# Optimization experiments

Measured on AMD Instinct MI355X. Metric: run time of the kernel, lower is better.

The kernel has to match this reference:

```python
import jax, jax.numpy as jnp
import numpy as np

B, H, W = 2, 64, 64
D = 256  # in_channels
EPS = 1e-5


def conv2d(x, w, pad):
    # x: NCHW, w: OIHW
    return jax.lax.conv_general_dilated(
        x, w, window_strides=(1, 1), padding=[(pad, pad), (pad, pad)],
        dimension_numbers=("NCHW", "OIHW", "NCHW"))


def code_projection(X, codewords, scale):
    # X: [B, D, H, W]; codewords: [K, D]; scale: [D, K]
    b, d = X.shape[0], X.shape[1]
    x = X.reshape(b, d, -1).transpose(0, 2, 1)              # [B, N, D]
    # residual: [B, N, D, K] (large broadcast tensor, as in the original)
    residual = (x[:, :, :, None] - codewords.T[None, None]) * scale
    Q = jax.nn.softmax(-0.5 * jnp.sum(residual ** 2, axis=2), axis=-1)  # [B, N, K]
    Z_num = jnp.einsum("bnk,bndk->bdk", Q, residual)        # sum over N
    Z_ = Z_num / Q.sum(axis=1)[:, None, :]                  # [B, D, K]
    Z = Z_ / jnp.sqrt(jnp.sum(Z_ ** 2, axis=1, keepdims=True))  # L2 over D
    return Z, Q


def graph_conv(inp, weight, gamma, beta):
    # inp: [B, D, K]
    adj = jnp.einsum("bdk,bdl->bkl", inp, inp)              # input^T @ input
    support = jnp.einsum("ij,bjk->bik", weight, inp)        # weight @ input
    out = jnp.einsum("bdk,bkl->bdl", support, adj)          # support @ adj
    out = jax.nn.relu(out)
    # BatchNorm1d (training-mode batch stats over (B, K) per channel D)
    mean = out.mean(axis=(0, 2), keepdims=True)
    var = out.var(axis=(0, 2), keepdims=True)
    return gamma[None, :, None] * (out - mean) / jnp.sqrt(var + EPS) + beta[None, :, None]


def reproj(graph, Q, h, w):
    # graph: [B, D, K], Q: [B, N, K]
    x = jnp.einsum("bdk,bnk->bdn", graph, Q)
    return x.reshape(graph.shape[0], graph.shape[1], h, w)


def branch(c, conv_w, cw, sc, gcnw, g, bta, ext_w, h, w):
    z, q = code_projection(conv2d(c, conv_w, 1), cw, sc)
    z = graph_conv(z, gcnw, g, bta)
    return conv2d(reproj(z, q, h, w), ext_w, 0) + c


def setup_inputs() -> dict:
    key = jax.random.key(0)
    keys = iter(jax.random.split(key, 64))
    nk = lambda: next(keys)
    inp = {}
    inp["c3"] = jax.random.normal(nk(), (B, 512, H, W), jnp.float32)
    inp["c4"] = jax.random.normal(nk(), (B, 512, H, W), jnp.float32)
    inp["c5"] = jax.random.normal(nk(), (B, 512, H, W), jnp.float32)
    for name, K in [("32", 32), ("16", 16), ("8", 8)]:
        inp[f"conv{name}_w"] = jax.random.normal(nk(), (256, 512, 3, 3), jnp.float32) * 0.02
        std1 = 1.0 / np.sqrt(K * D)
        inp[f"cw{name}"] = jax.random.uniform(nk(), (K, D), jnp.float32, -std1, std1)
        inp[f"sc{name}"] = jax.random.uniform(nk(), (D, K), jnp.float32, -1.0, 0.0)
        stdv = 1.0 / np.sqrt(D)
        inp[f"gcnw{name}"] = jax.random.uniform(nk(), (D, D), jnp.float32, -stdv, stdv)
        inp[f"bng{name}"] = jax.random.uniform(nk(), (D,), jnp.float32, 0.5, 1.5)
        inp[f"bnb{name}"] = jax.random.normal(nk(), (D,), jnp.float32) * 0.1
        inp[f"ext{name}_w"] = jax.random.normal(nk(), (512, 256, 1, 1), jnp.float32) * 0.05
    inp["smooth_w"] = jax.random.normal(nk(), (512, 1536, 3, 3), jnp.float32) * 0.01
    inp["smg"] = jax.random.uniform(nk(), (512,), jnp.float32, 0.5, 1.5)
    inp["smb"] = jax.random.normal(nk(), (512,), jnp.float32) * 0.1
    return inp


def reference(c3, c4, c5,
              conv32_w, cw32, sc32, gcnw32, bng32, bnb32, ext32_w,
              conv16_w, cw16, sc16, gcnw16, bng16, bnb16, ext16_w,
              conv8_w, cw8, sc8, gcnw8, bng8, bnb8, ext8_w,
              smooth_w, smg, smb):
    h, w = c3.shape[2], c3.shape[3]
    x_32 = branch(c3, conv32_w, cw32, sc32, gcnw32, bng32, bnb32, ext32_w, h, w)
    x_16 = branch(c4, conv16_w, cw16, sc16, gcnw16, bng16, bnb16, ext16_w, h, w)
    x_8 = branch(c5, conv8_w, cw8, sc8, gcnw8, bng8, bnb8, ext8_w, h, w)
    out = jnp.concatenate([x_8, x_16, x_32], axis=1)        # [B, 1536, H, W]
    out = conv2d(out, smooth_w, 1)
    # BatchNorm2d (training-mode batch stats) + ReLU
    mean = out.mean(axis=(0, 2, 3), keepdims=True)
    var = out.var(axis=(0, 2, 3), keepdims=True)
    out = smg[None, :, None, None] * (out - mean) / jnp.sqrt(var + EPS) + smb[None, :, None, None]
    return jax.nn.relu(out)
```

## Files before the change

kernel.cpp:

```cpp
#include <hip/hip_runtime.h>
#include <hip/hip_bf16.h>
#include <math.h>

#define HWN 4096
#define DCH 256
#define EPSV 1e-5f

typedef unsigned short u16;
typedef __attribute__((ext_vector_type(8))) short short8b;
typedef __attribute__((ext_vector_type(4))) float fx4;
typedef __attribute__((ext_vector_type(8))) unsigned short u16x8;

static __device__ inline u16 f2bf(float f) {
  __hip_bfloat16 h = __float2bfloat16(f);
  return *reinterpret_cast<u16*>(&h);
}
static __device__ inline float bf2f(u16 u) {
  unsigned int v = ((unsigned int)u) << 16;
  return __uint_as_float(v);
}

__global__ __launch_bounds__(256) void t_chwc3_k(const float* __restrict__ i0p,
    const float* __restrict__ i1p, const float* __restrict__ i2p,
    u16* __restrict__ out) {
  __shared__ float tl[32][257];
  const int p0 = blockIdx.x * 256, cic = blockIdx.y;
  const int z = blockIdx.z;
  const int br = z >> 1, b = z & 1;
  const float* in = (br == 0) ? i0p : ((br == 1) ? i1p : i2p);
  const int t = threadIdx.x;
  const float* ip = in + ((size_t)(b * 512 + cic * 32)) * HWN + p0;
#pragma unroll
  for (int r = 0; r < 32; ++r) tl[r][t] = ip[(size_t)r * HWN + t];
  __syncthreads();
  u16* op = out + ((size_t)((z * 16 + cic)) * HWN + p0 + t) * 32;
#pragma unroll
  for (int g = 0; g < 4; ++g) {
    u16x8 o;
#pragma unroll
    for (int j = 0; j < 8; ++j) o[j] = f2bf(tl[g * 8 + j][t]);
    *reinterpret_cast<u16x8*>(op + g * 8) = o;
  }
}

template<int CIN, int COUT>
__global__ __launch_bounds__(256) void wpack_k(const float* __restrict__ w0,
    const float* __restrict__ w1, const float* __restrict__ w2,
    u16* __restrict__ wp) {
  constexpr int NCIC = CIN / 32, NCOG = COUT / 16;
  const int br = blockIdx.y;
  const float* w = (br == 0) ? w0 : ((br == 1) ? w1 : w2);
  u16* wpb = wp + (size_t)br * 9 * NCIC * NCOG * 512;
  const int cog = blockIdx.x % NCOG, cic = blockIdx.x / NCOG;
  __shared__ float ws_[16 * 32 * 9];
  const int t = threadIdx.x;
  const float* src = w + ((size_t)(cog * 16) * CIN + cic * 32) * 9;
  for (int i = t; i < 4608; i += 256) {
    int co = i / 288, r = i % 288;
    ws_[i] = src[(size_t)co * CIN * 9 + r];
  }
  __syncthreads();
  const size_t tapstride = (size_t)NCIC * NCOG * 512;
  const size_t base = ((size_t)cic * NCOG + cog) * 512;
#pragma unroll
  for (int tap = 0; tap < 9; ++tap) {
#pragma unroll
    for (int e0 = 0; e0 < 512; e0 += 256) {
      int e = e0 + t;
      int kg = e >> 7, m = (e >> 3) & 15, j = e & 7;
      wpb[tap * tapstride + base + e] = f2bf(ws_[m * 288 + (kg * 8 + j) * 9 + tap]);
    }
  }
}

template<int CIN, int COUT, int SPLIT, int COW, int WPE, bool BF16OUT>
__global__ __launch_bounds__(256, WPE) void convlds3_k(
    const u16* __restrict__ xt, const u16* __restrict__ wp,
    void* __restrict__ outv) {
  constexpr int NCIC = CIN / 32;
  constexpr int NCO = COUT / COW;
  constexpr int NWT = COW / 16;
  constexpr int CICPS = NCIC / SPLIT;
  constexpr int NST = CICPS * 3;
  constexpr int TAPB = COW * 32;
  constexpr int WSH = TAPB / 4;
  constexpr int RNDS = WSH / 512;
  constexpr int PXS = 40;
  constexpr int AROW = 66 * PXS;
  constexpr size_t OUTEL = (size_t)2 * COUT * HWN;
  __shared__ u16 bl[3 * TAPB];
  __shared__ u16 al[6 * AROW];

  const int br = blockIdx.y;
  xt += (size_t)br * 2 * NCIC * HWN * 32;
  wp += (size_t)br * 9 * NCIC * (COUT / 16) * 512;

  int g = blockIdx.x;
  const int cpx = (int)gridDim.x >> 3;
  g = (g & 7) * cpx + (g >> 3);
  const int s = g / (32 * NCO);
  const int rem = g % (32 * NCO);
  const int rt = rem / NCO;
  const int cob = (rem % NCO) * COW;

  const int wv = threadIdx.x >> 6, lane = threadIdx.x & 63;
  const int b = (rt * 4) >> 6;
  const int h0 = (rt * 4) & 63;
  const int h = h0 + wv;
  const int m = lane & 15, kg = lane >> 4;
  const int cic0 = s * CICPS;
  const int t = threadIdx.x;

  fx4 acc[4][NWT];
#pragma unroll
  for (int i = 0; i < 4; ++i)
#pragma unroll
    for (int jn = 0; jn < NWT; ++jn) acc[i][jn] = (fx4){0.f, 0.f, 0.f, 0.f};

  const u16x8 zero16 = (u16x8){0, 0, 0, 0, 0, 0, 0, 0};
  const int lds_lane = wv * WSH + lane * 8;
  const int a_px = t >> 2, a_sl = t & 3;
  const int a_wr = (a_px + 1) * PXS + a_sl * 8;

  auto load_a = [&](int cic, u16x8* dst) {
    const u16* xc = xt + ((size_t)(b * NCIC + cic)) * HWN * 32;
#pragma unroll
    for (int r = 0; r < 6; ++r) {
      const int hl = h0 - 1 + r;
      u16x8 v = zero16;
      if ((unsigned)hl < 64u)
        v = *reinterpret_cast<const u16x8*>(xc + (size_t)hl * 2048 + t * 8);
      dst[r] = v;
    }
  };
  auto write_a = [&](const u16x8* src) {
#pragma unroll
    for (int r = 0; r < 6; ++r)
      *reinterpret_cast<u16x8*>(&al[r * AROW + a_wr]) = src[r];
  };

  if (t < 48) {
    int r = t >> 3, side = (t >> 2) & 1, sl = t & 3;
    *reinterpret_cast<u16x8*>(&al[r * AROW + (side ? 65 * PXS : 0) + sl * 8]) = zero16;
  }
  {
    u16x8 a0[6];
    load_a(cic0, a0);
    write_a(a0);
#pragma unroll
    for (int t3 = 0; t3 < 3; ++t3) {
      const u16* srcb = wp + (((size_t)t3 * NCIC + cic0) * (COUT / 16) + (cob >> 4)) * 512;
#pragma unroll
      for (int r = 0; r < RNDS; ++r)
        *reinterpret_cast<u16x8*>(&bl[t3 * TAPB + lds_lane + r * 512]) =
            *reinterpret_cast<const u16x8*>(srcb + lds_lane + r * 512);
    }
  }
  __syncthreads();

#pragma unroll 1
  for (int st = 0; st < NST; ++st) {
    const bool hasnext = (st + 1 < NST);
    const int ty = st % 3;
    const bool newcic = hasnext && (ty == 2);
    u16x8 stg[3][RNDS];
    u16x8 astg[6];
    if (hasnext) {
      const int cicn = cic0 + (st + 1) / 3, tyn = (st + 1) % 3;
#pragma unroll
      for (int t3 = 0; t3 < 3; ++t3) {
        const int tap = tyn * 3 + t3;
        const u16* srcb = wp + (((size_t)tap * NCIC + cicn) * (COUT / 16) + (cob >> 4)) * 512;
#pragma unroll
        for (int r = 0; r < RNDS; ++r)
          stg[t3][r] = *reinterpret_cast<const u16x8*>(srcb + lds_lane + r * 512);
      }
      if (newcic) load_a(cicn, astg);
    }
    const u16* arow = al + (wv + ty) * AROW + kg * 8;
#pragma unroll
    for (int tx = 0; tx < 3; ++tx) {
      short8b a[4];
#pragma unroll
      for (int mt = 0; mt < 4; ++mt)
        a[mt] = *reinterpret_cast<const short8b*>(arow + (mt * 16 + m + tx) * PXS);
      short8b bb[NWT];
#pragma unroll
      for (int nt = 0; nt < NWT; ++nt)
        bb[nt] = *reinterpret_cast<const short8b*>(&bl[tx * TAPB + nt * 512 + lane * 8]);
#pragma unroll
      for (int mt = 0; mt < 4; ++mt)
#pragma unroll
        for (int nt = 0; nt < NWT; ++nt)
          acc[mt][nt] = __builtin_amdgcn_mfma_f32_16x16x32_bf16(a[mt], bb[nt], acc[mt][nt], 0, 0, 0);
    }
    __syncthreads();
    if (hasnext) {
      if (newcic) write_a(astg);
#pragma unroll
      for (int t3 = 0; t3 < 3; ++t3)
#pragma unroll
        for (int r = 0; r < RNDS; ++r)
          *reinterpret_cast<u16x8*>(&bl[t3 * TAPB + lds_lane + r * 512]) = stg[t3][r];
      __syncthreads();
    }
  }

#pragma unroll
  for (int mt = 0; mt < 4; ++mt)
#pragma unroll
    for (int nt = 0; nt < NWT; ++nt) {
      int co = cob + nt * 16 + m;
      size_t idx = ((size_t)(b * COUT + co)) * HWN + h * 64 + mt * 16 + kg * 4;
      if (BF16OUT) {
        u16* op = (u16*)outv + (size_t)(br * SPLIT + s) * OUTEL + idx;
        ushort4 o;
        o.x = f2bf(acc[mt][nt][0]); o.y = f2bf(acc[mt][nt][1]);
        o.z = f2bf(acc[mt][nt][2]); o.w = f2bf(acc[mt][nt][3]);
        *reinterpret_cast<ushort4*>(op) = o;
      } else {
        float* op = (float*)outv + (size_t)(br * SPLIT + s) * OUTEL + idx;
        *reinterpret_cast<fx4*>(op) = acc[mt][nt];
      }
    }
}

__global__ __launch_bounds__(256) void bnall_k(const u16* __restrict__ slab,
    float* __restrict__ dout, const float* __restrict__ gm,
    const float* __restrict__ bt) {
  const int o = blockIdx.x;
  const size_t el = (size_t)2 * 512 * HWN;
  const int t = threadIdx.x;
  float y[2][2][8];
  float s = 0.f, ss = 0.f;
#pragma unroll
  for (int b = 0; b < 2; ++b)
#pragma unroll
    for (int c = 0; c < 2; ++c) {
      const size_t base = ((size_t)(b * 512 + o)) * HWN + c * 2048 + t * 8;
      u16x8 v0 = *reinterpret_cast<const u16x8*>(slab + base);
      u16x8 v1 = *reinterpret_cast<const u16x8*>(slab + el + base);
      u16x8 v2 = *reinterpret_cast<const u16x8*>(slab + 2 * el + base);
      u16x8 v3 = *reinterpret_cast<const u16x8*>(slab + 3 * el + base);
#pragma unroll
      for (int j = 0; j < 8; ++j) {
        float yv = (bf2f(v0[j]) + bf2f(v1[j])) + (bf2f(v2[j]) + bf2f(v3[j]));
        y[b][c][j] = yv; s += yv; ss = fmaf(yv, yv, ss);
      }
    }
  __shared__ float rs[4], rss[4], fin[2];
  for (int off = 32; off; off >>= 1) { s += __shfl_down(s, off); ss += __shfl_down(ss, off); }
  int lane = t & 63, wid = t >> 6;
  if (lane == 0) { rs[wid] = s; rss[wid] = ss; }
  __syncthreads();
  if (t == 0) {
    float S = rs[0] + rs[1] + rs[2] + rs[3];
    float SS = rss[0] + rss[1] + rss[2] + rss[3];
    float mean = S / (2 * HWN);
    float var = SS / (2 * HWN) - mean * mean;
    fin[0] = mean;
    fin[1] = 1.f / sqrtf(var + EPSV);
  }
  __syncthreads();
  const float mean = fin[0], giv = fin[1] * gm[o], be = bt[o];
#pragma unroll
  for (int b = 0; b < 2; ++b)
#pragma unroll
    for (int c = 0; c < 2; ++c) {
      const size_t base = ((size_t)(b * 512 + o)) * HWN + c * 2048 + t * 8;
      fx4 o0, o1;
#pragma unroll
      for (int j = 0; j < 4; ++j)
        o0[j] = fmaxf(fmaf(y[b][c][j] - mean, giv, be), 0.f);
#pragma unroll
      for (int j = 0; j < 4; ++j)
        o1[j] = fmaxf(fmaf(y[b][c][4 + j] - mean, giv, be), 0.f);
      *reinterpret_cast<fx4*>(dout + base) = o0;
      *reinterpret_cast<fx4*>(dout + base + 4) = o1;
    }
}

__global__ __launch_bounds__(256) void prep3_k(
    const float* __restrict__ sc0, const float* __restrict__ sc1, const float* __restrict__ sc2,
    const float* __restrict__ cw0, const float* __restrict__ cw1, const float* __restrict__ cw2,
    float2* __restrict__ AB, float* __restrict__ Ck) {
  const int br = blockIdx.y;
  const int K = 8 << br;
  const int k = blockIdx.x;
  if (k >= K) return;
  const float* sc = (br == 0) ? sc0 : ((br == 1) ? sc1 : sc2);
  const float* cw = (br == 0) ? cw0 : ((br == 1) ? cw1 : cw2);
  float2* ABb = AB + 2048 * ((1 << br) - 1);
  float* Ckb = Ck + 8 * ((1 << br) - 1);
  const int d = threadIdx.x;
  float s = sc[d * K + k];
  float a = s * s;
  float c = cw[k * DCH + d];
  ABb[d * K + k] = make_float2(a, c * a);
  float tt = c * s;
  tt = tt * tt;
  __shared__ float red[4];
  for (int off = 32; off; off >>= 1) tt += __shfl_down(tt, off);
  int lane = threadIdx.x & 63, wid = threadIdx.x >> 6;
  if (lane == 0) red[wid] = tt;
  __syncthreads();
  if (threadIdx.x == 0) Ckb[k] = red[0] + red[1] + red[2] + red[3];
}

template<int K>
static __device__ void score_body(int b, float* sm,
    const u16* __restrict__ s0p, const u16* __restrict__ s1p,
    const float2* __restrict__ AB, const float* __restrict__ Ck,
    float* __restrict__ Qt, float* __restrict__ Qsp) {
  const int lane = threadIdx.x & 63;
  const int g = threadIdx.x >> 6;
  const int n = blockIdx.x * 64 + lane;
  const size_t bbase = ((size_t)b * DCH) * HWN + n;
  float s_[K];
#pragma unroll
  for (int k = 0; k < K; ++k) s_[k] = 0.f;
  for (int d = g * 64; d < g * 64 + 64; ++d) {
    const size_t ofs = bbase + (size_t)d * HWN;
    float xv = bf2f(s0p[ofs]) + bf2f(s1p[ofs]);
    float x2 = xv * xv;
    float xm = -2.f * xv;
    const float2* abp = AB + d * K;
#pragma unroll
    for (int k = 0; k < K; ++k) {
      float2 ab = abp[k];
      s_[k] = fmaf(x2, ab.x, s_[k]);
      s_[k] = fmaf(xm, ab.y, s_[k]);
    }
  }
  float* smr = sm + (g * 64 + lane) * (K + 1);
#pragma unroll
  for (int k = 0; k < K; ++k) smr[k] = s_[k];
  __syncthreads();
  if (g == 0) {
    const float* r0 = sm + lane * (K + 1);
    const float* r1 = sm + (64 + lane) * (K + 1);
    const float* r2 = sm + (128 + lane) * (K + 1);
    const float* r3 = sm + (192 + lane) * (K + 1);
    float mx = -1e30f;
#pragma unroll
    for (int k = 0; k < K; ++k) {
      float v = (r0[k] + r1[k]) + (r2[k] + r3[k]);
      s_[k] = -0.5f * (v + Ck[k]);
      mx = fmaxf(mx, s_[k]);
    }
    float sum = 0.f;
#pragma unroll
    for (int k = 0; k < K; ++k) { float e = expf(s_[k] - mx); s_[k] = e; sum += e; }
    float inv = 1.f / sum;
#pragma unroll
    for (int k = 0; k < K; ++k) {
      float v = s_[k] * inv;
      Qt[((size_t)(b * K + k)) * HWN + n] = v;
      for (int off = 32; off; off >>= 1) v += __shfl_down(v, off);
      if (lane == 0) Qsp[((size_t)(b * K + k)) * 64 + blockIdx.x] = v;
    }
  }
}

__global__ __launch_bounds__(256) void score3_k(const u16* __restrict__ bslab,
    const float2* __restrict__ AB3, const float* __restrict__ Ck3,
    float* __restrict__ Qt3, float* __restrict__ Qsp3) {
  __shared__ float sm[4 * 64 * 33];
  const int z = blockIdx.y, br = z >> 1, b = z & 1;
  const size_t XEL = (size_t)2 * DCH * HWN;
  const u16* s0 = bslab + (size_t)br * 2 * XEL;
  const u16* s1 = s0 + XEL;
  if (br == 0)
    score_body<8>(b, sm, s0, s1, AB3, Ck3, Qt3, Qsp3);
  else if (br == 1)
    score_body<16>(b, sm, s0, s1, AB3 + 2048, Ck3 + 8, Qt3 + 65536, Qsp3 + 1024);
  else
    score_body<32>(b, sm, s0, s1, AB3 + 6144, Ck3 + 24, Qt3 + 196608, Qsp3 + 3072);
}

template<int K>
static __device__ void mmulp_body(int b, float* xs, float* pw,
    const u16* __restrict__ s0p, const u16* __restrict__ s1p,
    const float* __restrict__ Qt, float* __restrict__ Mp) {
  const int d = blockIdx.x, nch = blockIdx.y;
  const int t = threadIdx.x;
  const size_t ofs = ((size_t)(b * DCH + d)) * HWN + nch * 512 + t;
  xs[t] = bf2f(s0p[ofs]) + bf2f(s1p[ofs]);
  xs[t + 256] = bf2f(s0p[ofs + 256]) + bf2f(s1p[ofs + 256]);
  __syncthreads();
  const int lane = t & 63, wid = t >> 6;
#pragma unroll
  for (int k = 0; k < K; ++k) {
    const float* qp = Qt + ((size_t)(b * K + k)) * HWN + nch * 512;
    float s = fmaf(xs[t], qp[t], xs[t + 256] * qp[t + 256]);
    for (int off = 32; off; off >>= 1) s += __shfl_down(s, off);
    if (lane == 0) pw[wid * 33 + k] = s;
  }
  __syncthreads();
  if (t < K)
    Mp[(((size_t)(b * DCH + d)) * K + t) * 8 + nch] =
        (pw[t] + pw[33 + t]) + (pw[66 + t] + pw[99 + t]);
}

__global__ __launch_bounds__(256) void mmulp3_k(const u16* __restrict__ bslab,
    const float* __restrict__ Qt3, float* __restrict__ Mp3) {
  __shared__ float xs[512];
  __shared__ float pw[4 * 33];
  const int z = blockIdx.z, br = z >> 1, b = z & 1;
  const size_t XEL = (size_t)2 * DCH * HWN;
  const u16* s0 = bslab + (size_t)br * 2 * XEL;
  const u16* s1 = s0 + XEL;
  if (br == 0)
    mmulp_body<8>(b, xs, pw, s0, s1, Qt3, Mp3);
  else if (br == 1)
    mmulp_body<16>(b, xs, pw, s0, s1, Qt3 + 65536, Mp3 + 32768);
  else
    mmulp_body<32>(b, xs, pw, s0, s1, Qt3 + 196608, Mp3 + 98304);
}

template<int K>
static __device__ void fuse1_body(int b, float* buf, const float* __restrict__ Mp,
    const float* __restrict__ Qsp, const float* __restrict__ sc,
    const float* __restrict__ cw, const float* __restrict__ Wm,
    float* __restrict__ Graw) {
  float* zl = buf;
  float* adj = zl + DCH * K;
  float* rn = adj + K * K;
  float* qsl = rn + K;
  const int t = threadIdx.x;
  if (t < K) {
    const float* qp = Qsp + ((size_t)(b * K + t)) * 64;
    float s = 0.f;
    for (int i = 0; i < 64; ++i) s += qp[i];
    qsl[t] = s;
  }
  __syncthreads();
#pragma unroll
  for (int k = 0; k < K; ++k) {
    const float* mp = Mp + (((size_t)(b * DCH + t)) * K + k) * 8;
    fx4 p0 = *reinterpret_cast<const fx4*>(mp);
    fx4 p1 = *reinterpret_cast<const fx4*>(mp + 4);
    float mm = ((p0[0] + p0[1]) + (p0[2] + p0[3])) + ((p1[0] + p1[1]) + (p1[2] + p1[3]));
    float qs = qsl[k];
    zl[t * K + k] = sc[t * K + k] * (mm - cw[k * DCH + t] * qs) / qs;
  }
  __syncthreads();
  if (t < K) {
    float s = 0.f;
    for (int i = 0; i < DCH; ++i) { float v = zl[i * K + t]; s = fmaf(v, v, s); }
    rn[t] = 1.f / sqrtf(s);
  }
  __syncthreads();
#pragma unroll
  for (int k = 0; k < K; ++k) zl[t * K + k] *= rn[k];
  __syncthreads();
  for (int p = t; p < K * K; p += 256) {
    int k = p / K, l = p % K;
    float s = 0.f;
    for (int i = 0; i < DCH; ++i) s = fmaf(zl[i * K + k], zl[i * K + l], s);
    adj[p] = s;
  }
  __syncthreads();
  float sup[K];
#pragma unroll
  for (int k = 0; k < K; ++k) sup[k] = 0.f;
  const float* wr = Wm + (size_t)t * DCH;
  for (int jj = 0; jj < DCH; ++jj) {
    float wv = wr[jj];
#pragma unroll
    for (int k = 0; k < K; ++k) sup[k] = fmaf(wv, zl[jj * K + k], sup[k]);
  }
#pragma unroll
  for (int l = 0; l < K; ++l) {
    float s = 0.f;
#pragma unroll
    for (int k = 0; k < K; ++k) s = fmaf(sup[k], adj[k * K + l], s);
    Graw[((size_t)(b * DCH + t)) * K + l] = fmaxf(s, 0.f);
  }
}

__global__ __launch_bounds__(256) void fuse13_k(const float* __restrict__ Mp3,
    const float* __restrict__ Qsp3,
    const float* __restrict__ sc0, const float* __restrict__ sc1, const float* __restrict__ sc2,
    const float* __restrict__ cw0, const float* __restrict__ cw1, const float* __restrict__ cw2,
    const float* __restrict__ wm0, const float* __restrict__ wm1, const float* __restrict__ wm2,
    float* __restrict__ Graw3) {
  __shared__ float buf[DCH * 32 + 32 * 32 + 64];
  const int z = blockIdx.x, br = z >> 1, b = z & 1;
  if (br == 0)
    fuse1_body<8>(b, buf, Mp3, Qsp3, sc0, cw0, wm0, Graw3);
  else if (br == 1)
    fuse1_body<16>(b, buf, Mp3 + 32768, Qsp3 + 1024, sc1, cw1, wm1, Graw3 + 4096);
  else
    fuse1_body<32>(b, buf, Mp3 + 98304, Qsp3 + 3072, sc2, cw2, wm2, Graw3 + 12288);
}

template<int K>
static __device__ void fuse2_body(int b, int ob, float* gl,
    const float* __restrict__ Graw, const float* __restrict__ gamma,
    const float* __restrict__ beta, const float* __restrict__ E,
    float* __restrict__ EG) {
  const int t = threadIdx.x;
  {
    const int d = t;
    float s = 0.f, ss = 0.f;
#pragma unroll
    for (int b2 = 0; b2 < 2; ++b2)
#pragma unroll
      for (int l = 0; l < K; ++l) {
        float v = Graw[((size_t)(b2 * DCH + d)) * K + l];
        s += v; ss = fmaf(v, v, ss);
      }
    const float invn = 1.f / (2 * K);
    float mean = s * invn;
    float var  = ss * invn - mean * mean;
    float giv  = gamma[d] / sqrtf(var + EPSV);
    float be   = beta[d];
#pragma unroll
    for (int l = 0; l < K; ++l) {
      float v = Graw[((size_t)(b * DCH + d)) * K + l];
      gl[d * K + l] = fmaf(v - mean, giv, be);
    }
  }
  __syncthreads();
  const int o = ob * 256 + t;
  float a[K];
#pragma unroll
  for (int k = 0; k < K; ++k) a[k] = 0.f;
  const fx4* e4 = reinterpret_cast<const fx4*>(E + (size_t)o * DCH);
  for (int d4 = 0; d4 < 64; ++d4) {
    fx4 v = e4[d4];
#pragma unroll
    for (int j = 0; j < 4; ++j) {
      float vv = v[j];
#pragma unroll
      for (int k = 0; k < K; ++k)
        a[k] = fmaf(vv, gl[(d4 * 4 + j) * K + k], a[k]);
    }
  }
#pragma unroll
  for (int k = 0; k < K; ++k)
    EG[((size_t)(b * 512 + o)) * K + k] = a[k];
}

__global__ __launch_bounds__(256) void fuse23_k(const float* __restrict__ Graw3,
    const float* __restrict__ g0, const float* __restrict__ g1, const float* __restrict__ g2,
    const float* __restrict__ b0, const float* __restrict__ b1, const float* __restrict__ b2,
    const float* __restrict__ e0, const float* __restrict__ e1, const float* __restrict__ e2,
    float* __restrict__ EG3) {
  __shared__ float gl[DCH * 32];
  const int b = blockIdx.x, ob = blockIdx.y, br = blockIdx.z;
  if (br == 0)
    fuse2_body<8>(b, ob, gl, Graw3, g0, b0, e0, EG3);
  else if (br == 1)
    fuse2_body<16>(b, ob, gl, Graw3 + 4096, g1, b1, e1, EG3 + 8192);
  else
    fuse2_body<32>(b, ob, gl, Graw3 + 12288, g2, b2, e2, EG3 + 24576);
}

template<int K>
static __device__ void yout_body(int b, u16* egl, const float* __restrict__ EG,
    const float* __restrict__ Qt, const float* __restrict__ cres,
    u16* __restrict__ cat, int coff) {
  const int cg = blockIdx.y;
  const int t = threadIdx.x;
  const int lane = t & 63, sub = t >> 6;
  const int n = blockIdx.x * 64 + lane;
  for (int i = t; i < K * 128; i += 256) {
    int k = i >> 7, co = i & 127;
    egl[i] = f2bf(EG[((size_t)(b * 512 + cg * 128 + co)) * K + k]);
  }
  float q[K];
#pragma unroll
  for (int k = 0; k < K; ++k) q[k] = Qt[((size_t)(b * K + k)) * HWN + n];
  __syncthreads();
  const float* crow = cres + (size_t)b * 512 * HWN + n;
#pragma unroll
  for (int it = 0; it < 4; ++it) {
    int co = sub * 32 + it * 8;
    int gco = cg * 128 + co;
    float y[8];
#pragma unroll
    for (int jj = 0; jj < 8; ++jj) y[jj] = crow[(size_t)(gco + jj) * HWN];
#pragma unroll
    for (int k = 0; k < K; ++k) {
      u16x8 eg = *reinterpret_cast<const u16x8*>(&egl[k * 128 + co]);
#pragma unroll
      for (int jj = 0; jj < 8; ++jj) y[jj] = fmaf(bf2f(eg[jj]), q[k], y[jj]);
    }
    u16x8 o;
#pragma unroll
    for (int jj = 0; jj < 8; ++jj) o[jj] = f2bf(y[jj]);
    int ch = coff + gco;
    *reinterpret_cast<u16x8*>(cat +
        (((size_t)(b * 48 + (ch >> 5)) * HWN + n) * 32 + (ch & 31))) = o;
  }
}

__global__ __launch_bounds__(256) void yout3_k(const float* __restrict__ EG3,
    const float* __restrict__ Qt3, const float* __restrict__ c5,
    const float* __restrict__ c4, const float* __restrict__ c3,
    u16* __restrict__ cat) {
  __shared__ u16 egl[32 * 128];
  const int z = blockIdx.z, br = z >> 1, b = z & 1;
  if (br == 0)
    yout_body<8>(b, egl, EG3, Qt3, c5, cat, 0);
  else if (br == 1)
    yout_body<16>(b, egl, EG3 + 8192, Qt3 + 65536, c4, cat, 512);
  else
    yout_body<32>(b, egl, EG3 + 24576, Qt3 + 196608, c3, cat, 1024);
}

extern "C" void kernel_launch(void* const* d_in, const int* in_sizes, int n_in,
                              void* d_out, int out_size, void* d_ws, size_t ws_size,
                              hipStream_t stream) {
  const float* c3 = (const float*)d_in[0];
  const float* c4 = (const float*)d_in[1];
  const float* c5 = (const float*)d_in[2];
  const float* smooth_w = (const float*)d_in[24];
  const float* smg = (const float*)d_in[25];
  const float* smb = (const float*)d_in[26];
  float* dout = (float*)d_out;

  char* wsb = (char*)d_ws;
  u16* Xt3 = (u16*)wsb;
  u16* cat = (u16*)wsb;
  u16* Wb  = (u16*)(wsb + 25165824);
  float* pool  = (float*)(wsb + 39321600);
  char* C = wsb + 43540480;
  u16* bslab   = (u16*)C;
  u16* sslab   = (u16*)C;

  float* Qt3  = pool;
  float* Qsp3 = pool + 458752;
  float* Mp3  = pool + 465920;
  float* Graw3 = pool + 723968;
  float* EG3  = pool + 752640;
  float2* AB3 = (float2*)(pool + 809984);
  float* Ck3  = pool + 838656;

  t_chwc3_k<<<dim3(16, 16, 6), 256, 0, stream>>>(c5, c4, c3, Xt3);
  wpack_k<512, 256><<<dim3(256, 3), 256, 0, stream>>>(
      (const float*)d_in[17], (const float*)d_in[10], (const float*)d_in[3], Wb);
  convlds3_k<512, 256, 2, 64, 3, true><<<dim3(256, 3), 256, 0, stream>>>(Xt3, Wb, bslab);

  prep3_k<<<dim3(32, 3), 256, 0, stream>>>(
      (const float*)d_in[19], (const float*)d_in[12], (const float*)d_in[5],
      (const float*)d_in[18], (const float*)d_in[11], (const float*)d_in[4],
      AB3, Ck3);
  score3_k<<<dim3(64, 6), 256, 0, stream>>>(bslab, AB3, Ck3, Qt3, Qsp3);
  mmulp3_k<<<dim3(256, 8, 6), 256, 0, stream>>>(bslab, Qt3, Mp3);
  fuse13_k<<<6, 256, 0, stream>>>(Mp3, Qsp3,
      (const float*)d_in[19], (const float*)d_in[12], (const float*)d_in[5],
      (const float*)d_in[18], (const float*)d_in[11], (const float*)d_in[4],
      (const float*)d_in[20], (const float*)d_in[13], (const float*)d_in[6],
      Graw3);
  fuse23_k<<<dim3(2, 2, 3), 256, 0, stream>>>(Graw3,
      (const float*)d_in[21], (const float*)d_in[14], (const float*)d_in[7],
      (const float*)d_in[22], (const float*)d_in[15], (const float*)d_in[8],
      (const float*)d_in[23], (const float*)d_in[16], (const float*)d_in[9],
      EG3);
  yout3_k<<<dim3(64, 4, 6), 256, 0, stream>>>(EG3, Qt3, c5, c4, c3, cat);

  wpack_k<1536, 512><<<dim3(1536, 1), 256, 0, stream>>>(smooth_w, smooth_w, smooth_w, Wb);
  convlds3_k<1536, 512, 4, 128, 2, true><<<dim3(512, 1), 256, 0, stream>>>(cat, Wb, sslab);
  bnall_k<<<512, 256, 0, stream>>>(sslab, dout, smg, smb);
}
```

Measured before the change: 431.4 us.

## Use wider output tiles with four-way K split and unpadded LDS activation rows

The branch conv now runs with a four-way input-channel split and 128-wide output-channel tiles instead of a two-way split and 64-wide tiles. Score and mmulp kernels sum four partial slabs instead of two to match. The LDS activation layout also drops the 40-element pixel stride padding in favour of a dense 32-element stride with a small row pad. The aim is more weight reuse per block, at the cost of more partial-sum traffic, possible LDS bank conflicts and lower occupancy.

```diff
diff --git a/kernel.cpp b/kernel.cpp
--- a/kernel.cpp
+++ b/kernel.cpp
@@ -74,7 +74,7 @@
 }
 
 template<int CIN, int COUT, int SPLIT, int COW, int WPE, bool BF16OUT>
-__global__ __launch_bounds__(256, WPE) void convlds3_k(
+__global__ __launch_bounds__(256, WPE) void convlds4_k(
     const u16* __restrict__ xt, const u16* __restrict__ wp,
     void* __restrict__ outv) {
   constexpr int NCIC = CIN / 32;
@@ -85,8 +85,7 @@
   constexpr int TAPB = COW * 32;
   constexpr int WSH = TAPB / 4;
   constexpr int RNDS = WSH / 512;
-  constexpr int PXS = 40;
-  constexpr int AROW = 66 * PXS;
+  constexpr int AROW = 66 * 32 + 8;
   constexpr size_t OUTEL = (size_t)2 * COUT * HWN;
   __shared__ u16 bl[3 * TAPB];
   __shared__ u16 al[6 * AROW];
@@ -119,8 +118,6 @@
 
   const u16x8 zero16 = (u16x8){0, 0, 0, 0, 0, 0, 0, 0};
   const int lds_lane = wv * WSH + lane * 8;
-  const int a_px = t >> 2, a_sl = t & 3;
-  const int a_wr = (a_px + 1) * PXS + a_sl * 8;
 
   auto load_a = [&](int cic, u16x8* dst) {
     const u16* xc = xt + ((size_t)(b * NCIC + cic)) * HWN * 32;
@@ -136,12 +133,12 @@
   auto write_a = [&](const u16x8* src) {
 #pragma unroll
     for (int r = 0; r < 6; ++r)
-      *reinterpret_cast<u16x8*>(&al[r * AROW + a_wr]) = src[r];
+      *reinterpret_cast<u16x8*>(&al[r * AROW + 32 + t * 8]) = src[r];
   };
 
   if (t < 48) {
     int r = t >> 3, side = (t >> 2) & 1, sl = t & 3;
-    *reinterpret_cast<u16x8*>(&al[r * AROW + (side ? 65 * PXS : 0) + sl * 8]) = zero16;
+    *reinterpret_cast<u16x8*>(&al[r * AROW + (side ? 65 * 32 : 0) + sl * 8]) = zero16;
   }
   {
     u16x8 a0[6];
@@ -183,7 +180,7 @@
       short8b a[4];
 #pragma unroll
       for (int mt = 0; mt < 4; ++mt)
-        a[mt] = *reinterpret_cast<const short8b*>(arow + (mt * 16 + m + tx) * PXS);
+        a[mt] = *reinterpret_cast<const short8b*>(arow + (mt * 16 + m + tx) * 32);
       short8b bb[NWT];
 #pragma unroll
       for (int nt = 0; nt < NWT; ++nt)
@@ -308,10 +305,10 @@
 }
 
 template<int K>
-static __device__ void score_body(int b, float* sm,
-    const u16* __restrict__ s0p, const u16* __restrict__ s1p,
+static __device__ void score_body(int b, float* sm, const u16* __restrict__ sl,
     const float2* __restrict__ AB, const float* __restrict__ Ck,
     float* __restrict__ Qt, float* __restrict__ Qsp) {
+  const size_t XEL = (size_t)2 * DCH * HWN;
   const int lane = threadIdx.x & 63;
   const int g = threadIdx.x >> 6;
   const int n = blockIdx.x * 64 + lane;
@@ -321,7 +318,8 @@
   for (int k = 0; k < K; ++k) s_[k] = 0.f;
   for (int d = g * 64; d < g * 64 + 64; ++d) {
     const size_t ofs = bbase + (size_t)d * HWN;
-    float xv = bf2f(s0p[ofs]) + bf2f(s1p[ofs]);
+    float xv = (bf2f(sl[ofs]) + bf2f(sl[XEL + ofs]))
+             + (bf2f(sl[2 * XEL + ofs]) + bf2f(sl[3 * XEL + ofs]));
     float x2 = xv * xv;
     float xm = -2.f * xv;
     const float2* abp = AB + d * K;
@@ -368,25 +366,27 @@
   __shared__ float sm[4 * 64 * 33];
   const int z = blockIdx.y, br = z >> 1, b = z & 1;
   const size_t XEL = (size_t)2 * DCH * HWN;
-  const u16* s0 = bslab + (size_t)br * 2 * XEL;
-  const u16* s1 = s0 + XEL;
+  const u16* sl = bslab + (size_t)br * 4 * XEL;
   if (br == 0)
-    score_body<8>(b, sm, s0, s1, AB3, Ck3, Qt3, Qsp3);
+    score_body<8>(b, sm, sl, AB3, Ck3, Qt3, Qsp3);
   else if (br == 1)
-    score_body<16>(b, sm, s0, s1, AB3 + 2048, Ck3 + 8, Qt3 + 65536, Qsp3 + 1024);
+    score_body<16>(b, sm, sl, AB3 + 2048, Ck3 + 8, Qt3 + 65536, Qsp3 + 1024);
   else
-    score_body<32>(b, sm, s0, s1, AB3 + 6144, Ck3 + 24, Qt3 + 196608, Qsp3 + 3072);
+    score_body<32>(b, sm, sl, AB3 + 6144, Ck3 + 24, Qt3 + 196608, Qsp3 + 3072);
 }
 
 template<int K>
 static __device__ void mmulp_body(int b, float* xs, float* pw,
-    const u16* __restrict__ s0p, const u16* __restrict__ s1p,
-    const float* __restrict__ Qt, float* __restrict__ Mp) {
+    const u16* __restrict__ sl, const float* __restrict__ Qt,
+    float* __restrict__ Mp) {
+  const size_t XEL = (size_t)2 * DCH * HWN;
   const int d = blockIdx.x, nch = blockIdx.y;
   const int t = threadIdx.x;
   const size_t ofs = ((size_t)(b * DCH + d)) * HWN + nch * 512 + t;
-  xs[t] = bf2f(s0p[ofs]) + bf2f(s1p[ofs]);
-  xs[t + 256] = bf2f(s0p[ofs + 256]) + bf2f(s1p[ofs + 256]);
+  xs[t] = (bf2f(sl[ofs]) + bf2f(sl[XEL + ofs]))
+        + (bf2f(sl[2 * XEL + ofs]) + bf2f(sl[3 * XEL + ofs]));
+  xs[t + 256] = (bf2f(sl[ofs + 256]) + bf2f(sl[XEL + ofs + 256]))
+              + (bf2f(sl[2 * XEL + ofs + 256]) + bf2f(sl[3 * XEL + ofs + 256]));
   __syncthreads();
   const int lane = t & 63, wid = t >> 6;
 #pragma unroll
@@ -408,14 +408,13 @@
   __shared__ float pw[4 * 33];
   const int z = blockIdx.z, br = z >> 1, b = z & 1;
   const size_t XEL = (size_t)2 * DCH * HWN;
-  const u16* s0 = bslab + (size_t)br * 2 * XEL;
-  const u16* s1 = s0 + XEL;
+  const u16* sl = bslab + (size_t)br * 4 * XEL;
   if (br == 0)
-    mmulp_body<8>(b, xs, pw, s0, s1, Qt3, Mp3);
+    mmulp_body<8>(b, xs, pw, sl, Qt3, Mp3);
   else if (br == 1)
-    mmulp_body<16>(b, xs, pw, s0, s1, Qt3 + 65536, Mp3 + 32768);
+    mmulp_body<16>(b, xs, pw, sl, Qt3 + 65536, Mp3 + 32768);
   else
-    mmulp_body<32>(b, xs, pw, s0, s1, Qt3 + 196608, Mp3 + 98304);
+    mmulp_body<32>(b, xs, pw, sl, Qt3 + 196608, Mp3 + 98304);
 }
 
 template<int K>
@@ -642,7 +641,7 @@
   t_chwc3_k<<<dim3(16, 16, 6), 256, 0, stream>>>(c5, c4, c3, Xt3);
   wpack_k<512, 256><<<dim3(256, 3), 256, 0, stream>>>(
       (const float*)d_in[17], (const float*)d_in[10], (const float*)d_in[3], Wb);
-  convlds3_k<512, 256, 2, 64, 3, true><<<dim3(256, 3), 256, 0, stream>>>(Xt3, Wb, bslab);
+  convlds4_k<512, 256, 4, 128, 2, true><<<dim3(256, 3), 256, 0, stream>>>(Xt3, Wb, bslab);
 
   prep3_k<<<dim3(32, 3), 256, 0, stream>>>(
       (const float*)d_in[19], (const float*)d_in[12], (const float*)d_in[5],
@@ -663,6 +662,6 @@
   yout3_k<<<dim3(64, 4, 6), 256, 0, stream>>>(EG3, Qt3, c5, c4, c3, cat);
 
   wpack_k<1536, 512><<<dim3(1536, 1), 256, 0, stream>>>(smooth_w, smooth_w, smooth_w, Wb);
-  convlds3_k<1536, 512, 4, 128, 2, true><<<dim3(512, 1), 256, 0, stream>>>(cat, Wb, sslab);
+  convlds4_k<1536, 512, 4, 128, 2, true><<<dim3(512, 1), 256, 0, stream>>>(cat, Wb, sslab);
   bnall_k<<<512, 256, 0, stream>>>(sslab, dout, smg, smb);
 }
```

Measured after the change: 443.4 us. 2.8% more time.
